# Optimization experiments

Measured on AMD Instinct MI355X. Metric: run time of the kernel, lower is better.

The kernel has to match this reference:

```python
import jax, jax.numpy as jnp
import numpy as np

NUM_CATEGORIES = 64
INPUT_DIM = 256
HIDDEN_DIM = 256
N = 4096  # number of samples (each with its own category)
M = 16    # rows per sample


def setup_inputs() -> dict:
    key = jax.random.key(0)
    k_x, k_cat, k_W = jax.random.split(key, 3)
    x = jax.random.normal(k_x, (N, M, INPUT_DIM), dtype=jnp.float32)
    cat_ids = jax.random.randint(k_cat, (N,), 0, NUM_CATEGORIES, dtype=jnp.int64)
    W = 0.02 * jax.random.normal(k_W, (NUM_CATEGORIES, INPUT_DIM, HIDDEN_DIM), dtype=jnp.float32)
    b = jnp.zeros((NUM_CATEGORIES, HIDDEN_DIM), dtype=jnp.float32)
    return {"x": x, "cat_ids": cat_ids, "W": W, "b": b}


def reference(x, cat_ids, W, b):
    # Gather per-sample weights/biases, then batched matmul + bias add.
    selected_W = W[cat_ids]              # [N, input_dim, hidden_dim]
    selected_b = b[cat_ids]              # [N, hidden_dim]
    out = jnp.einsum('nmi,nih->nmh', x, selected_W) + selected_b[:, None, :]
    return out
```

## Files before the change

### kernel.cpp

```cpp
#include <hip/hip_runtime.h>
#include <hip/hip_bf16.h>
#include <stdint.h>

#define N_SAMPLES 4096
#define M_ROWS 16
#define K_DIM 256
#define H_DIM 256
#define N_CATS 64
#define SPB 4
#define MAX_PADDED (N_SAMPLES + N_CATS * (SPB - 1))
#define NGROUP (MAX_PADDED / SPB)
#define GPX (NGROUP / 8)
#define GEMM_GRID (NGROUP * 2)
#define AROW 264

typedef _Float16 half8 __attribute__((ext_vector_type(8)));
typedef _Float16 half4 __attribute__((ext_vector_type(4)));
typedef float floatx4 __attribute__((ext_vector_type(4)));

#define GLOAD_LDS(g, l)                                          \
  __builtin_amdgcn_global_load_lds(                              \
      (const __attribute__((address_space(1))) void*)(g),        \
      (__attribute__((address_space(3))) void*)(l), 16, 0, 0)

#define WT_BYTES  ((size_t)N_CATS * K_DIM * H_DIM * 2)
#define X16_BYTES ((size_t)N_SAMPLES * M_ROWS * K_DIM * 2)
#define GCAT_OFF_F (WT_BYTES + X16_BYTES)
#define ORD_OFF_F  (GCAT_OFF_F + 4288)
#define WS_NEED_F  (ORD_OFF_F + (size_t)MAX_PADDED * 4)
#define GCAT_OFF_S WT_BYTES
#define ORD_OFF_S  (WT_BYTES + 4288)
#define WS_NEED_S  (ORD_OFF_S + (size_t)MAX_PADDED * 4)

__global__ __launch_bounds__(256)
void prep_combined(const float* __restrict__ W, _Float16* __restrict__ Wt,
                   const int* __restrict__ cat, int* __restrict__ ord,
                   int* __restrict__ gcat,
                   const float* __restrict__ x, _Float16* __restrict__ x16) {
  const int tid = threadIdx.x;
  const int bid = blockIdx.x;
  if (bid < 1024) {
    __shared__ _Float16 t[64][72];
    const int c  = bid >> 4;
    const int kb = (bid >> 2) & 3;
    const int hb = bid & 3;
    const int r  = tid >> 2;
    const int cg = (tid & 3) * 16;
    const float* src = W + ((size_t)c << 16) + (size_t)(kb * 64 + r) * 256 + hb * 64 + cg;
#pragma unroll
    for (int j = 0; j < 16; j += 4) {
      float4 v = *(const float4*)(src + j);
      t[r][cg + j + 0] = (_Float16)v.x;
      t[r][cg + j + 1] = (_Float16)v.y;
      t[r][cg + j + 2] = (_Float16)v.z;
      t[r][cg + j + 3] = (_Float16)v.w;
    }
    __syncthreads();
    _Float16* dst = Wt + ((size_t)c << 16) + (size_t)(hb * 64 + r) * 256 + kb * 64 + cg;
    half8 o0, o1;
#pragma unroll
    for (int j = 0; j < 8; j++) o0[j] = t[cg + j][r];
#pragma unroll
    for (int j = 0; j < 8; j++) o1[j] = t[cg + 8 + j][r];
    *(half8*)(dst) = o0;
    *(half8*)(dst + 8) = o1;
  } else if (bid == 1024) {
    __shared__ int hist[N_CATS];
    __shared__ int poffs[N_CATS];
    __shared__ int curs[N_CATS];
    if (tid < N_CATS) hist[tid] = 0;
    for (int i = tid; i < MAX_PADDED; i += 256) ord[i] = -1;
    for (int i = tid; i < NGROUP; i += 256) gcat[i] = 0;
    __syncthreads();
    for (int i = tid; i < N_SAMPLES; i += 256) atomicAdd(&hist[cat[i]], 1);
    __syncthreads();
    if (tid == 0) {
      int run = 0;
      for (int c = 0; c < N_CATS; c++) {
        poffs[c] = run;
        run += ((hist[c] + SPB - 1) / SPB) * SPB;
      }
    }
    if (tid < N_CATS) curs[tid] = 0;
    __syncthreads();
    if (tid < N_CATS) {
      const int c = tid;
      const int g0 = poffs[c] >> 2;
      const int ng = (hist[c] + SPB - 1) >> 2;
      for (int g = 0; g < ng; g++) gcat[g0 + g] = c;
    }
    for (int i = tid; i < N_SAMPLES; i += 256) {
      int c = cat[i];
      int p = poffs[c] + atomicAdd(&curs[c], 1);
      ord[p] = i;
    }
  } else {
    const int s = bid - 1025;
    const float* src = x + ((size_t)s << 12);
    _Float16* dst = x16 + ((size_t)s << 12);
#pragma unroll
    for (int it = 0; it < 4; it++) {
      const int r = it * 4 + (tid >> 6);
      const int c = (tid & 63) << 2;
      float4 v = *(const float4*)(src + r * 256 + c);
      half4 h;
      h[0] = (_Float16)v.x; h[1] = (_Float16)v.y;
      h[2] = (_Float16)v.z; h[3] = (_Float16)v.w;
      const int slot = c >> 3;
      *(half4*)(dst + r * 256 + (((slot ^ (r & 7)) << 3) | (c & 7))) = h;
    }
  }
}

__global__ __launch_bounds__(256, 4)
void gemm_dma(const _Float16* __restrict__ x16, const float* __restrict__ bias,
              const _Float16* __restrict__ Wt, const int* __restrict__ ord,
              const int* __restrict__ gcat, float* __restrict__ out) {
  __shared__ __align__(16) _Float16 sA[64 * 256];

  const int tid = threadIdx.x;
  const int B = blockIdx.x;
  const int xcd = B & 7;
  const int slot = B >> 3;
  const int h_half = slot & 1;
  const int group = xcd * GPX + (slot >> 1);
  const int h0 = h_half << 7;

  const int cat = gcat[group];
  const int4 sm = *(const int4*)(ord + group * 4);
  if (sm.x < 0) return;

  const int wid  = tid >> 6;
  const int lane = tid & 63;
  const int l15  = lane & 15;
  const int quad = lane >> 4;

  const _Float16* wb = Wt + ((size_t)cat << 16) +
                       (size_t)(h0 + wid * 32 + l15) * K_DIM + quad * 8;

  half8 bf[5][2];
#pragma unroll
  for (int kt = 0; kt < 4; kt++) {
    bf[kt][0] = *(const half8*)(wb + kt * 32);
    bf[kt][1] = *(const half8*)(wb + 16 * K_DIM + kt * 32);
  }
  const float bv0 = bias[cat * H_DIM + h0 + wid * 32 + l15];
  const float bv1 = bias[cat * H_DIM + h0 + wid * 32 + 16 + l15];
  __builtin_amdgcn_sched_barrier(0);

  const int smp0 = (wid == 0) ? sm.x : (wid == 1) ? sm.y : (wid == 2) ? sm.z : sm.w;
  const int smp  = (smp0 >= 0) ? smp0 : sm.x;
  const _Float16* asrc = x16 + ((size_t)smp << 12) + (lane << 3);
  _Float16* adst = sA + wid * 4096;
#pragma unroll
  for (int i = 0; i < 8; i++)
    GLOAD_LDS(asrc + i * 512, adst + i * 512);

  floatx4 acc[4][2];
#pragma unroll
  for (int i = 0; i < 4; i++)
#pragma unroll
    for (int j = 0; j < 2; j++)
#pragma unroll
      for (int e = 0; e < 4; e++) acc[i][j][e] = 0.0f;

  __syncthreads();

#pragma unroll
  for (int kt = 0; kt < 8; kt++) {
    if (kt < 4) {
      bf[(kt + 4) % 5][0] = *(const half8*)(wb + (kt + 4) * 32);
      bf[(kt + 4) % 5][1] = *(const half8*)(wb + 16 * K_DIM + (kt + 4) * 32);
      __builtin_amdgcn_sched_barrier(0);
    }
    half8 af[4];
#pragma unroll
    for (int mt = 0; mt < 4; mt++)
      af[mt] = *(const half8*)&sA[(size_t)(mt * 16 + l15) * 256 +
                                  (((kt * 4 + quad) ^ (l15 & 7)) << 3)];
#pragma unroll
    for (int mt = 0; mt < 4; mt++) {
      acc[mt][0] = __builtin_amdgcn_mfma_f32_16x16x32_f16(af[mt], bf[kt % 5][0], acc[mt][0], 0, 0, 0);
      acc[mt][1] = __builtin_amdgcn_mfma_f32_16x16x32_f16(af[mt], bf[kt % 5][1], acc[mt][1], 0, 0, 0);
    }
  }

  const int srow[4] = {sm.x, sm.y, sm.z, sm.w};
#pragma unroll
  for (int mt = 0; mt < 4; mt++) {
    const int s = srow[mt];
    if (s < 0) continue;
    float* obase = out + ((size_t)s << 12);
#pragma unroll
    for (int nt = 0; nt < 2; nt++) {
      const int col = h0 + wid * 32 + nt * 16 + l15;
      const float bv = nt ? bv1 : bv0;
#pragma unroll
      for (int rr = 0; rr < 4; rr++) {
        const int row = quad * 4 + rr;
        obase[(size_t)row * H_DIM + col] = acc[mt][nt][rr] + bv;
      }
    }
  }
}

__global__ __launch_bounds__(256, 3)
void gemm_small(const float* __restrict__ x, const float* __restrict__ bias,
                const _Float16* __restrict__ Wt, const int* __restrict__ ord,
                const int* __restrict__ gcat, float* __restrict__ out) {
  __shared__ __align__(16) _Float16 sA[64 * AROW];

  const int tid = threadIdx.x;
  const int B = blockIdx.x;
  const int xcd = B & 7;
  const int slot = B >> 3;
  const int h_half = slot & 1;
  const int group = xcd * GPX + (slot >> 1);
  const int h0 = h_half << 7;

  const int cat = gcat[group];
  const int4 sm = *(const int4*)(ord + group * 4);
  if (sm.x < 0) return;

  const int wid  = tid >> 6;
  const int lane = tid & 63;
  const int l15  = lane & 15;
  const int quad = lane >> 4;

  const _Float16* wb = Wt + ((size_t)cat << 16) +
                       (size_t)(h0 + wid * 32 + l15) * K_DIM + quad * 8;

  half8 bf[5][2];
#pragma unroll
  for (int kt = 0; kt < 4; kt++) {
    bf[kt][0] = *(const half8*)(wb + kt * 32);
    bf[kt][1] = *(const half8*)(wb + 16 * K_DIM + kt * 32);
  }
  const float bv0 = bias[cat * H_DIM + h0 + wid * 32 + l15];
  const float bv1 = bias[cat * H_DIM + h0 + wid * 32 + 16 + l15];
  __builtin_amdgcn_sched_barrier(0);

  const int smp = (wid == 0) ? sm.x : (wid == 1) ? sm.y : (wid == 2) ? sm.z : sm.w;
  const float* asrc = (smp >= 0) ? (x + ((size_t)smp << 12)) : nullptr;
  _Float16* adst = sA + (size_t)(wid * 16) * AROW;
  if (asrc) {
#pragma unroll
    for (int j = 0; j < 16; j++) {
      float4 v = *(const float4*)(asrc + j * 256 + lane * 4);
      half4 h;
      h[0] = (_Float16)v.x; h[1] = (_Float16)v.y;
      h[2] = (_Float16)v.z; h[3] = (_Float16)v.w;
      *(half4*)(adst + (size_t)j * AROW + lane * 4) = h;
    }
  } else {
    half4 h;
#pragma unroll
    for (int e = 0; e < 4; e++) h[e] = (_Float16)0.0f;
#pragma unroll
    for (int j = 0; j < 16; j++)
      *(half4*)(adst + (size_t)j * AROW + lane * 4) = h;
  }

  floatx4 acc[4][2];
#pragma unroll
  for (int i = 0; i < 4; i++)
#pragma unroll
    for (int j = 0; j < 2; j++)
#pragma unroll
      for (int e = 0; e < 4; e++) acc[i][j][e] = 0.0f;

  __syncthreads();

#pragma unroll
  for (int kt = 0; kt < 8; kt++) {
    if (kt < 4) {
      bf[(kt + 4) % 5][0] = *(const half8*)(wb + (kt + 4) * 32);
      bf[(kt + 4) % 5][1] = *(const half8*)(wb + 16 * K_DIM + (kt + 4) * 32);
      __builtin_amdgcn_sched_barrier(0);
    }
    half8 af[4];
#pragma unroll
    for (int mt = 0; mt < 4; mt++)
      af[mt] = *(const half8*)&sA[(size_t)(mt * 16 + l15) * AROW + kt * 32 + quad * 8];
#pragma unroll
    for (int mt = 0; mt < 4; mt++) {
      acc[mt][0] = __builtin_amdgcn_mfma_f32_16x16x32_f16(af[mt], bf[kt % 5][0], acc[mt][0], 0, 0, 0);
      acc[mt][1] = __builtin_amdgcn_mfma_f32_16x16x32_f16(af[mt], bf[kt % 5][1], acc[mt][1], 0, 0, 0);
    }
  }

  const int srow[4] = {sm.x, sm.y, sm.z, sm.w};
#pragma unroll
  for (int mt = 0; mt < 4; mt++) {
    const int s = srow[mt];
    if (s < 0) continue;
    float* obase = out + ((size_t)s << 12);
#pragma unroll
    for (int nt = 0; nt < 2; nt++) {
      const int col = h0 + wid * 32 + nt * 16 + l15;
      const float bv = nt ? bv1 : bv0;
#pragma unroll
      for (int rr = 0; rr < 4; rr++) {
        const int row = quad * 4 + rr;
        obase[(size_t)row * H_DIM + col] = acc[mt][nt][rr] + bv;
      }
    }
  }
}

__global__ __launch_bounds__(256)
void naive_kernel(const float* __restrict__ x, const int* __restrict__ cat,
                  const float* __restrict__ W, const float* __restrict__ bias,
                  float* __restrict__ out) {
  __shared__ float sx[16 * 256];
  const int n = blockIdx.x;
  const int tid = threadIdx.x;
  const int c = cat[n];
  const float* xs = x + (size_t)n * 16 * 256;
  for (int i = tid; i < 16 * 256; i += 256) sx[i] = xs[i];
  __syncthreads();
  const float* Wc = W + ((size_t)c << 16);
  float accv[16];
  float bv = bias[c * 256 + tid];
#pragma unroll
  for (int m = 0; m < 16; m++) accv[m] = bv;
  for (int k = 0; k < 256; k++) {
    float w = Wc[(size_t)k * 256 + tid];
#pragma unroll
    for (int m = 0; m < 16; m++) accv[m] += sx[m * 256 + k] * w;
  }
#pragma unroll
  for (int m = 0; m < 16; m++) out[((size_t)n * 16 + m) * 256 + tid] = accv[m];
}

extern "C" void kernel_launch(void* const* d_in, const int* in_sizes, int n_in,
                              void* d_out, int out_size, void* d_ws, size_t ws_size,
                              hipStream_t stream) {
  const float* x    = (const float*)d_in[0];
  const int*   cat  = (const int*)d_in[1];
  const float* W    = (const float*)d_in[2];
  const float* bias = (const float*)d_in[3];
  float* out = (float*)d_out;

  char* ws = (char*)d_ws;
  if (ws_size >= WS_NEED_F) {
    _Float16* Wt  = (_Float16*)ws;
    _Float16* x16 = (_Float16*)(ws + WT_BYTES);
    int* gcat = (int*)(ws + GCAT_OFF_F);
    int* ord  = (int*)(ws + ORD_OFF_F);
    prep_combined<<<1025 + N_SAMPLES, 256, 0, stream>>>(W, Wt, cat, ord, gcat, x, x16);
    gemm_dma<<<GEMM_GRID, 256, 0, stream>>>(x16, bias, Wt, ord, gcat, out);
  } else if (ws_size >= WS_NEED_S) {
    _Float16* Wt = (_Float16*)ws;
    int* gcat = (int*)(ws + GCAT_OFF_S);
    int* ord  = (int*)(ws + ORD_OFF_S);
    prep_combined<<<1025, 256, 0, stream>>>(W, Wt, cat, ord, gcat, x, nullptr);
    gemm_small<<<GEMM_GRID, 256, 0, stream>>>(x, bias, Wt, ord, gcat, out);
  } else {
    naive_kernel<<<N_SAMPLES, 256, 0, stream>>>(x, cat, W, bias, out);
  }
}
```

Before: 159.7 us.

## Compute both hidden halves per block to reuse the staged A tile

```diff
diff --git a/kernel.cpp b/kernel.cpp
--- a/kernel.cpp
+++ b/kernel.cpp
@@ -112,7 +112,7 @@
   }
 }
 
-__global__ __launch_bounds__(256, 4)
+__global__ __launch_bounds__(256, 3)
 void gemm_dma(const _Float16* __restrict__ x16, const float* __restrict__ bias,
               const _Float16* __restrict__ Wt, const int* __restrict__ ord,
               const int* __restrict__ gcat, float* __restrict__ out) {
@@ -121,10 +121,7 @@
   const int tid = threadIdx.x;
   const int B = blockIdx.x;
   const int xcd = B & 7;
-  const int slot = B >> 3;
-  const int h_half = slot & 1;
-  const int group = xcd * GPX + (slot >> 1);
-  const int h0 = h_half << 7;
+  const int group = xcd * GPX + (B >> 3);
 
   const int cat = gcat[group];
   const int4 sm = *(const int4*)(ord + group * 4);
@@ -135,17 +132,22 @@
   const int l15  = lane & 15;
   const int quad = lane >> 4;
 
-  const _Float16* wb = Wt + ((size_t)cat << 16) +
-                       (size_t)(h0 + wid * 32 + l15) * K_DIM + quad * 8;
+  const _Float16* wb0 = Wt + ((size_t)cat << 16) +
+                        (size_t)(wid * 32 + l15) * K_DIM + quad * 8;
+  const _Float16* wb1 = wb0 + (size_t)128 * K_DIM;
 
   half8 bf[5][2];
 #pragma unroll
   for (int kt = 0; kt < 4; kt++) {
-    bf[kt][0] = *(const half8*)(wb + kt * 32);
-    bf[kt][1] = *(const half8*)(wb + 16 * K_DIM + kt * 32);
-  }
-  const float bv0 = bias[cat * H_DIM + h0 + wid * 32 + l15];
-  const float bv1 = bias[cat * H_DIM + h0 + wid * 32 + 16 + l15];
+    bf[kt][0] = *(const half8*)(wb0 + kt * 32);
+    bf[kt][1] = *(const half8*)(wb0 + 16 * K_DIM + kt * 32);
+  }
+  float bv[2][2];
+#pragma unroll
+  for (int p = 0; p < 2; p++)
+#pragma unroll
+    for (int nt = 0; nt < 2; nt++)
+      bv[p][nt] = bias[cat * H_DIM + p * 128 + wid * 32 + nt * 16 + l15];
   __builtin_amdgcn_sched_barrier(0);
 
   const int smp0 = (wid == 0) ? sm.x : (wid == 1) ? sm.y : (wid == 2) ? sm.z : sm.w;
@@ -166,13 +168,19 @@
 
   __syncthreads();
 
-#pragma unroll
-  for (int kt = 0; kt < 8; kt++) {
-    if (kt < 4) {
-      bf[(kt + 4) % 5][0] = *(const half8*)(wb + (kt + 4) * 32);
-      bf[(kt + 4) % 5][1] = *(const half8*)(wb + 16 * K_DIM + (kt + 4) * 32);
+  const int srow[4] = {sm.x, sm.y, sm.z, sm.w};
+
+#pragma unroll
+  for (int g = 0; g < 16; g++) {
+    if (g < 12) {
+      const int gn = g + 4;
+      const _Float16* wbn = (gn < 8) ? wb0 : wb1;
+      const int ktn = gn & 7;
+      bf[gn % 5][0] = *(const half8*)(wbn + ktn * 32);
+      bf[gn % 5][1] = *(const half8*)(wbn + 16 * K_DIM + ktn * 32);
       __builtin_amdgcn_sched_barrier(0);
     }
+    const int kt = g & 7;
     half8 af[4];
 #pragma unroll
     for (int mt = 0; mt < 4; mt++)
@@ -180,12 +188,33 @@
                                   (((kt * 4 + quad) ^ (l15 & 7)) << 3)];
 #pragma unroll
     for (int mt = 0; mt < 4; mt++) {
-      acc[mt][0] = __builtin_amdgcn_mfma_f32_16x16x32_f16(af[mt], bf[kt % 5][0], acc[mt][0], 0, 0, 0);
-      acc[mt][1] = __builtin_amdgcn_mfma_f32_16x16x32_f16(af[mt], bf[kt % 5][1], acc[mt][1], 0, 0, 0);
-    }
-  }
-
-  const int srow[4] = {sm.x, sm.y, sm.z, sm.w};
+      acc[mt][0] = __builtin_amdgcn_mfma_f32_16x16x32_f16(af[mt], bf[g % 5][0], acc[mt][0], 0, 0, 0);
+      acc[mt][1] = __builtin_amdgcn_mfma_f32_16x16x32_f16(af[mt], bf[g % 5][1], acc[mt][1], 0, 0, 0);
+    }
+
+    if (g == 7) {
+#pragma unroll
+      for (int mt = 0; mt < 4; mt++) {
+        const int s = srow[mt];
+        if (s < 0) continue;
+        float* obase = out + ((size_t)s << 12);
+#pragma unroll
+        for (int nt = 0; nt < 2; nt++) {
+          const int col = wid * 32 + nt * 16 + l15;
+#pragma unroll
+          for (int rr = 0; rr < 4; rr++)
+            obase[(size_t)(quad * 4 + rr) * H_DIM + col] = acc[mt][nt][rr] + bv[0][nt];
+        }
+      }
+#pragma unroll
+      for (int i = 0; i < 4; i++)
+#pragma unroll
+        for (int j = 0; j < 2; j++)
+#pragma unroll
+          for (int e = 0; e < 4; e++) acc[i][j][e] = 0.0f;
+    }
+  }
+
 #pragma unroll
   for (int mt = 0; mt < 4; mt++) {
     const int s = srow[mt];
@@ -193,13 +222,10 @@
     float* obase = out + ((size_t)s << 12);
 #pragma unroll
     for (int nt = 0; nt < 2; nt++) {
-      const int col = h0 + wid * 32 + nt * 16 + l15;
-      const float bv = nt ? bv1 : bv0;
-#pragma unroll
-      for (int rr = 0; rr < 4; rr++) {
-        const int row = quad * 4 + rr;
-        obase[(size_t)row * H_DIM + col] = acc[mt][nt][rr] + bv;
-      }
+      const int col = 128 + wid * 32 + nt * 16 + l15;
+#pragma unroll
+      for (int rr = 0; rr < 4; rr++)
+        obase[(size_t)(quad * 4 + rr) * H_DIM + col] = acc[mt][nt][rr] + bv[1][nt];
     }
   }
 }
@@ -349,7 +375,7 @@
     int* gcat = (int*)(ws + GCAT_OFF_F);
     int* ord  = (int*)(ws + ORD_OFF_F);
     prep_combined<<<1025 + N_SAMPLES, 256, 0, stream>>>(W, Wt, cat, ord, gcat, x, x16);
-    gemm_dma<<<GEMM_GRID, 256, 0, stream>>>(x16, bias, Wt, ord, gcat, out);
+    gemm_dma<<<NGROUP, 256, 0, stream>>>(x16, bias, Wt, ord, gcat, out);
   } else if (ws_size >= WS_NEED_S) {
     _Float16* Wt = (_Float16*)ws;
     int* gcat = (int*)(ws + GCAT_OFF_S);
```

New measurement: 160.3 us. About the same (+0.4%).

## Fuse prep and grouped GEMM into one cooperative kernel with grid sync

Applied to the files above, without the earlier changes.

```diff
diff --git a/kernel.cpp b/kernel.cpp
--- a/kernel.cpp
+++ b/kernel.cpp
@@ -1,6 +1,9 @@
 #include <hip/hip_runtime.h>
+#include <hip/hip_cooperative_groups.h>
 #include <hip/hip_bf16.h>
 #include <stdint.h>
+
+namespace cg = cooperative_groups;
 
 #define N_SAMPLES 4096
 #define M_ROWS 16
@@ -13,6 +16,7 @@
 #define GPX (NGROUP / 8)
 #define GEMM_GRID (NGROUP * 2)
 #define AROW 264
+#define COOP_BLOCKS 1024
 
 typedef _Float16 half8 __attribute__((ext_vector_type(8)));
 typedef _Float16 half4 __attribute__((ext_vector_type(4)));
@@ -31,6 +35,183 @@
 #define GCAT_OFF_S WT_BYTES
 #define ORD_OFF_S  (WT_BYTES + 4288)
 #define WS_NEED_S  (ORD_OFF_S + (size_t)MAX_PADDED * 4)
+
+__global__ __launch_bounds__(256, 4)
+void fused_all(const float* __restrict__ x, const int* __restrict__ cat,
+               const float* __restrict__ W, const float* __restrict__ bias,
+               _Float16* __restrict__ Wt, _Float16* __restrict__ x16,
+               int* __restrict__ ord, int* __restrict__ gcat,
+               float* __restrict__ out) {
+  __shared__ __align__(16) _Float16 sA[64 * 256];
+  __shared__ int hist[N_CATS];
+  __shared__ int poffs[N_CATS];
+  __shared__ int curs[N_CATS];
+
+  const int tid  = threadIdx.x;
+  const int b    = blockIdx.x;
+  const int wid  = tid >> 6;
+  const int lane = tid & 63;
+  const int l15  = lane & 15;
+  const int quad = lane >> 4;
+
+  if (b == 0) {
+    if (tid < N_CATS) hist[tid] = 0;
+    for (int i = tid; i < MAX_PADDED; i += 256) ord[i] = -1;
+    for (int i = tid; i < NGROUP; i += 256) gcat[i] = 0;
+    __syncthreads();
+    for (int i = tid; i < N_SAMPLES; i += 256) atomicAdd(&hist[cat[i]], 1);
+    __syncthreads();
+    if (tid == 0) {
+      int run = 0;
+      for (int c = 0; c < N_CATS; c++) {
+        poffs[c] = run;
+        run += ((hist[c] + SPB - 1) / SPB) * SPB;
+      }
+    }
+    if (tid < N_CATS) curs[tid] = 0;
+    __syncthreads();
+    if (tid < N_CATS) {
+      const int c = tid;
+      const int g0 = poffs[c] >> 2;
+      const int ng = (hist[c] + SPB - 1) >> 2;
+      for (int g = 0; g < ng; g++) gcat[g0 + g] = c;
+    }
+    for (int i = tid; i < N_SAMPLES; i += 256) {
+      int c = cat[i];
+      int p = poffs[c] + atomicAdd(&curs[c], 1);
+      ord[p] = i;
+    }
+  }
+
+  {
+    _Float16 (*t)[72] = (_Float16(*)[72])sA;
+    const int c  = b >> 4;
+    const int kb = (b >> 2) & 3;
+    const int hb = b & 3;
+    const int r  = tid >> 2;
+    const int cg = (tid & 3) * 16;
+    const float* src = W + ((size_t)c << 16) + (size_t)(kb * 64 + r) * 256 + hb * 64 + cg;
+#pragma unroll
+    for (int j = 0; j < 16; j += 4) {
+      float4 v = *(const float4*)(src + j);
+      t[r][cg + j + 0] = (_Float16)v.x;
+      t[r][cg + j + 1] = (_Float16)v.y;
+      t[r][cg + j + 2] = (_Float16)v.z;
+      t[r][cg + j + 3] = (_Float16)v.w;
+    }
+    __syncthreads();
+    _Float16* dst = Wt + ((size_t)c << 16) + (size_t)(hb * 64 + r) * 256 + kb * 64 + cg;
+    half8 o0, o1;
+#pragma unroll
+    for (int j = 0; j < 8; j++) o0[j] = t[cg + j][r];
+#pragma unroll
+    for (int j = 0; j < 8; j++) o1[j] = t[cg + 8 + j][r];
+    *(half8*)(dst) = o0;
+    *(half8*)(dst + 8) = o1;
+  }
+
+  {
+    const int s = b * 4 + wid;
+    const float* src = x + ((size_t)s << 12);
+    _Float16* dst = x16 + ((size_t)s << 12);
+    const int cc = lane << 2;
+    const int slot = lane >> 1;
+    const int lo = cc & 7;
+#pragma unroll
+    for (int j = 0; j < 16; j++) {
+      float4 v = *(const float4*)(src + j * 256 + cc);
+      half4 h;
+      h[0] = (_Float16)v.x; h[1] = (_Float16)v.y;
+      h[2] = (_Float16)v.z; h[3] = (_Float16)v.w;
+      *(half4*)(dst + j * 256 + (((slot ^ (j & 7)) << 3) | lo)) = h;
+    }
+  }
+
+  __threadfence();
+  cg::this_grid().sync();
+  __threadfence();
+
+  for (int u = b; u < GEMM_GRID; u += COOP_BLOCKS) {
+    const int xcd = u & 7;
+    const int uslot = u >> 3;
+    const int h_half = uslot & 1;
+    const int group = xcd * GPX + (uslot >> 1);
+    const int h0 = h_half << 7;
+
+    const int catc = gcat[group];
+    const int4 sm = *(const int4*)(ord + group * 4);
+    __syncthreads();
+    if (sm.x < 0) continue;
+
+    const _Float16* wb = Wt + ((size_t)catc << 16) +
+                         (size_t)(h0 + wid * 32 + l15) * K_DIM + quad * 8;
+
+    half8 bf[5][2];
+#pragma unroll
+    for (int kt = 0; kt < 4; kt++) {
+      bf[kt][0] = *(const half8*)(wb + kt * 32);
+      bf[kt][1] = *(const half8*)(wb + 16 * K_DIM + kt * 32);
+    }
+    const float bv0 = bias[catc * H_DIM + h0 + wid * 32 + l15];
+    const float bv1 = bias[catc * H_DIM + h0 + wid * 32 + 16 + l15];
+    __builtin_amdgcn_sched_barrier(0);
+
+    const int smp0 = (wid == 0) ? sm.x : (wid == 1) ? sm.y : (wid == 2) ? sm.z : sm.w;
+    const int smp  = (smp0 >= 0) ? smp0 : sm.x;
+    const _Float16* asrc = x16 + ((size_t)smp << 12) + (lane << 3);
+    _Float16* adst = sA + wid * 4096;
+#pragma unroll
+    for (int i = 0; i < 8; i++)
+      GLOAD_LDS(asrc + i * 512, adst + i * 512);
+
+    floatx4 acc[4][2];
+#pragma unroll
+    for (int i = 0; i < 4; i++)
+#pragma unroll
+      for (int j = 0; j < 2; j++)
+#pragma unroll
+        for (int e = 0; e < 4; e++) acc[i][j][e] = 0.0f;
+
+    __syncthreads();
+
+#pragma unroll
+    for (int kt = 0; kt < 8; kt++) {
+      if (kt < 4) {
+        bf[(kt + 4) % 5][0] = *(const half8*)(wb + (kt + 4) * 32);
+        bf[(kt + 4) % 5][1] = *(const half8*)(wb + 16 * K_DIM + (kt + 4) * 32);
+        __builtin_amdgcn_sched_barrier(0);
+      }
+      half8 af[4];
+#pragma unroll
+      for (int mt = 0; mt < 4; mt++)
+        af[mt] = *(const half8*)&sA[(size_t)(mt * 16 + l15) * 256 +
+                                    (((kt * 4 + quad) ^ (l15 & 7)) << 3)];
+#pragma unroll
+      for (int mt = 0; mt < 4; mt++) {
+        acc[mt][0] = __builtin_amdgcn_mfma_f32_16x16x32_f16(af[mt], bf[kt % 5][0], acc[mt][0], 0, 0, 0);
+        acc[mt][1] = __builtin_amdgcn_mfma_f32_16x16x32_f16(af[mt], bf[kt % 5][1], acc[mt][1], 0, 0, 0);
+      }
+    }
+
+    const int srow[4] = {sm.x, sm.y, sm.z, sm.w};
+#pragma unroll
+    for (int mt = 0; mt < 4; mt++) {
+      const int s = srow[mt];
+      if (s < 0) continue;
+      float* obase = out + ((size_t)s << 12);
+#pragma unroll
+      for (int nt = 0; nt < 2; nt++) {
+        const int col = h0 + wid * 32 + nt * 16 + l15;
+        const float bv = nt ? bv1 : bv0;
+#pragma unroll
+        for (int rr = 0; rr < 4; rr++) {
+          const int row = quad * 4 + rr;
+          obase[(size_t)row * H_DIM + col] = acc[mt][nt][rr] + bv;
+        }
+      }
+    }
+  }
+}
 
 __global__ __launch_bounds__(256)
 void prep_combined(const float* __restrict__ W, _Float16* __restrict__ Wt,
@@ -348,8 +529,24 @@
     _Float16* x16 = (_Float16*)(ws + WT_BYTES);
     int* gcat = (int*)(ws + GCAT_OFF_F);
     int* ord  = (int*)(ws + ORD_OFF_F);
-    prep_combined<<<1025 + N_SAMPLES, 256, 0, stream>>>(W, Wt, cat, ord, gcat, x, x16);
-    gemm_dma<<<GEMM_GRID, 256, 0, stream>>>(x16, bias, Wt, ord, gcat, out);
+
+    int dev = 0;
+    hipGetDevice(&dev);
+    int coop = 0;
+    hipDeviceGetAttribute(&coop, hipDeviceAttributeCooperativeLaunch, dev);
+
+    hipError_t e = hipErrorUnknown;
+    if (coop) {
+      void* args[] = {(void*)&x, (void*)&cat, (void*)&W, (void*)&bias,
+                      (void*)&Wt, (void*)&x16, (void*)&ord, (void*)&gcat,
+                      (void*)&out};
+      e = hipLaunchCooperativeKernel((const void*)fused_all, dim3(COOP_BLOCKS),
+                                     dim3(256), args, 0, stream);
+    }
+    if (e != hipSuccess) {
+      prep_combined<<<1025 + N_SAMPLES, 256, 0, stream>>>(W, Wt, cat, ord, gcat, x, x16);
+      gemm_dma<<<GEMM_GRID, 256, 0, stream>>>(x16, bias, Wt, ord, gcat, out);
+    }
   } else if (ws_size >= WS_NEED_S) {
     _Float16* Wt = (_Float16*)ws;
     int* gcat = (int*)(ws + GCAT_OFF_S);
```

After: 506.4 us. +217.1%, slower.
